# Kernel tuning notes

Hardware: AMD Instinct MI355X
Metric: run time of the kernel (lower is better)

## Reference

```python
import jax, jax.numpy as jnp
import numpy as np

MAX_W = 32  # static upper bound on window length (= max(ends - begins) in the torch code)


def setup_inputs() -> dict:
    key = jax.random.key(0)
    k1, k2, k3 = jax.random.split(key, 3)
    B, T, D, S = 8, 4096, 256, 1024
    features = jax.random.normal(k1, (B, T, D), dtype=jnp.float32)
    begins = jax.random.randint(k2, (B, S), 0, T - MAX_W)
    wins = jax.random.randint(k3, (B, S), 1, MAX_W + 1)
    ends = begins + wins
    return {"features": features, "begins": begins, "ends": ends}


def reference(features, begins, ends):
    # Pooler(mode='mean', dropout_p=0.0) ragged branch: for each span s in batch b,
    # mean of features[b, begins[b,s]:ends[b,s], :] (empty spans -> 0, matching
    # F.embedding_bag mean on an empty bag).
    B, T, D = features.shape
    begins = jnp.maximum(begins, 0)  # clamp_min(0) as in torch code
    ends = jnp.maximum(ends, 0)
    pos = begins[..., None] + jnp.arange(MAX_W)        # [B, S, W]
    valid = pos < ends[..., None]                      # [B, S, W]
    idx = jnp.clip(pos, 0, T - 1)
    gathered = jax.vmap(lambda f, i: f[i])(features, idx)   # [B, S, W, D]
    summed = jnp.sum(jnp.where(valid[..., None], gathered, 0.0), axis=2)  # [B, S, D]
    count = valid.sum(-1).astype(features.dtype)       # [B, S]
    return summed / jnp.maximum(count, 1.0)[..., None]
```

## Files before the change

### kernel.cpp

```cpp
#include <hip/hip_runtime.h>
#include <hip/hip_bf16.h>


#define B_DIM 8
#define T_DIM 4096
#define D_DIM 256
#define S_DIM 1024
#define MAX_W 32
#define RWIDTH 128
#define NBLK (B_DIM * (T_DIM / RWIDTH))
#define STAGE_ROWS (RWIDTH + MAX_W - 1)
#define CAP 508

typedef float vfloat4 __attribute__((ext_vector_type(4)));
typedef const __attribute__((address_space(1))) uint32_t* gptr_t;
typedef __attribute__((address_space(3))) uint32_t* lptr_t;

struct SM {
    float rows[STAGE_ROWS][D_DIM];
    int count;
    unsigned short list[CAP];
};

__global__ __launch_bounds__(1024) void pooler_kernel(
    const float* __restrict__ features,
    const int*   __restrict__ begins,
    const int*   __restrict__ ends,
    float*       __restrict__ out)
{
    __shared__ SM sm;

    const int phys = blockIdx.x;
    const int b = phys & 7;
    const int r = phys >> 3;
    const int tid  = threadIdx.x;
    const int wv   = tid >> 6;
    const int lane = tid & 63;

    if (tid == 0) sm.count = 0;
    __syncthreads();

    const int row0  = r * RWIDTH;
    const int nrows = (T_DIM - row0) < STAGE_ROWS ? (T_DIM - row0) : STAGE_ROWS;
    const float* gbase = features + ((size_t)b * T_DIM + row0) * D_DIM + lane * 4;

    #pragma unroll
    for (int c = 0; c < (STAGE_ROWS + 15) / 16; ++c) {
        const int row = c * 16 + wv;
        if (row < nrows) {
            __builtin_amdgcn_global_load_lds(
                (gptr_t)(gbase + (size_t)row * D_DIM),
                (lptr_t)(&sm.rows[row][0]),
                16, 0, 0);
        }
    }

    {
        const int s  = tid;
        int bg = begins[b * S_DIM + s];
        int bgc = bg > 0 ? bg : 0;
        bgc = bgc < (T_DIM - 1) ? bgc : (T_DIM - 1);
        const bool pred = (bgc >> 7) == r;

        const unsigned long long mask = __ballot(pred);
        const int cnt = __popcll(mask);
        int base = 0;
        if (lane == 0 && cnt) base = atomicAdd(&sm.count, cnt);
        base = __shfl(base, 0);
        if (pred) {
            const int pos =
                base + __popcll(mask & ((1ULL << lane) - 1ULL));
            if (pos < CAP) {
                sm.list[pos] = (unsigned short)s;
            } else {
                int en = ends[b * S_DIM + s];
                int bb = bg > 0 ? bg : 0;
                en = en > 0 ? en : 0;
                en = en < T_DIM ? en : T_DIM;
                int w = en - bb;
                w = w < MAX_W ? w : MAX_W;
                float* op = out + (size_t)(b * S_DIM + s) * D_DIM;
                if (w <= 0) {
                    for (int d = 0; d < D_DIM; ++d) op[d] = 0.f;
                } else {
                    const float* fp =
                        features + ((size_t)b * T_DIM + bb) * D_DIM;
                    const float inv = 1.0f / (float)w;
                    for (int d = 0; d < D_DIM; ++d) {
                        float a = 0.f;
                        for (int j = 0; j < w; ++j) a += fp[(size_t)j * D_DIM + d];
                        op[d] = a * inv;
                    }
                }
            }
        }
    }

    __syncthreads();

    const int cnt = sm.count < CAP ? sm.count : CAP;
    for (int i = wv; i < cnt; i += 16) {
        const int s = sm.list[i];
        int bg = begins[b * S_DIM + s];
        int en = ends[b * S_DIM + s];
        bg = bg > 0 ? bg : 0;
        en = en > 0 ? en : 0;
        en = en < T_DIM ? en : T_DIM;
        int w = en - bg;
        w = w < MAX_W ? w : MAX_W;

        vfloat4* outp =
            reinterpret_cast<vfloat4*>(out + (size_t)(b * S_DIM + s) * D_DIM) + lane;

        if (w <= 0) {
            vfloat4 z = {0.f, 0.f, 0.f, 0.f};
            __builtin_nontemporal_store(z, outp);
            continue;
        }

        const int local = bg - row0;
        const vfloat4* lp =
            reinterpret_cast<const vfloat4*>(&sm.rows[local][0]) + lane;

        vfloat4 acc = {0.f, 0.f, 0.f, 0.f};
        #pragma unroll 8
        for (int j = 0; j < w; ++j) acc += lp[(size_t)j * (D_DIM / 4)];

        const float inv = 1.0f / (float)w;
        vfloat4 res = acc * inv;
        __builtin_nontemporal_store(res, outp);
    }
}

extern "C" void kernel_launch(void* const* d_in, const int* in_sizes, int n_in,
                              void* d_out, int out_size, void* d_ws, size_t ws_size,
                              hipStream_t stream) {
    const float* features = (const float*)d_in[0];
    const int*   begins   = (const int*)d_in[1];
    const int*   ends     = (const int*)d_in[2];
    float*       out      = (float*)d_out;

    pooler_kernel<<<NBLK, 1024, 0, stream>>>(features, begins, ends, out);
}
```

Before: 14.64 us.

## Split staged rows into two halves and overlap second load with first-half pooling

Stages the first 96 rows into LDS, then processes spans whose begin falls in the first 64 rows while the remaining rows load asynchronously. Spans are bucketed into two lists by half, with span id, local offset and width packed into each entry so the compute loop no longer re-reads begins/ends. The goal is to hide part of the global-to-LDS staging latency behind compute. In exchange it adds an extra barrier and vmcnt wait, and CAP shrinks to 120 per half, so a heavier half falls back to the slow per-thread global path more often.

```diff
diff --git a/kernel.cpp b/kernel.cpp
--- a/kernel.cpp
+++ b/kernel.cpp
@@ -10,7 +10,7 @@
 #define RWIDTH 128
 #define NBLK (B_DIM * (T_DIM / RWIDTH))
 #define STAGE_ROWS (RWIDTH + MAX_W - 1)
-#define CAP 508
+#define CAP 120
 
 typedef float vfloat4 __attribute__((ext_vector_type(4)));
 typedef const __attribute__((address_space(1))) uint32_t* gptr_t;
@@ -18,8 +18,8 @@
 
 struct SM {
     float rows[STAGE_ROWS][D_DIM];
-    int count;
-    unsigned short list[CAP];
+    int cnt[2];
+    unsigned int list[2][CAP];
 };
 
 __global__ __launch_bounds__(1024) void pooler_kernel(
@@ -37,7 +37,7 @@
     const int wv   = tid >> 6;
     const int lane = tid & 63;
 
-    if (tid == 0) sm.count = 0;
+    if (tid < 2) sm.cnt[tid] = 0;
     __syncthreads();
 
     const int row0  = r * RWIDTH;
@@ -45,87 +45,122 @@
     const float* gbase = features + ((size_t)b * T_DIM + row0) * D_DIM + lane * 4;
 
     #pragma unroll
-    for (int c = 0; c < (STAGE_ROWS + 15) / 16; ++c) {
-        const int row = c * 16 + wv;
-        if (row < nrows) {
-            __builtin_amdgcn_global_load_lds(
-                (gptr_t)(gbase + (size_t)row * D_DIM),
-                (lptr_t)(&sm.rows[row][0]),
-                16, 0, 0);
-        }
+    for (int k = 0; k < 6; ++k) {
+        const int row = wv + k * 16;
+        __builtin_amdgcn_global_load_lds(
+            (gptr_t)(gbase + (size_t)row * D_DIM),
+            (lptr_t)(&sm.rows[row][0]), 16, 0, 0);
     }
 
     {
-        const int s  = tid;
-        int bg = begins[b * S_DIM + s];
-        int bgc = bg > 0 ? bg : 0;
-        bgc = bgc < (T_DIM - 1) ? bgc : (T_DIM - 1);
+        const int s = tid;
+        const int bg = begins[b * S_DIM + s];
+        const int en = ends[b * S_DIM + s];
+        int begin = bg > 0 ? bg : 0;
+        int end   = en > 0 ? en : 0;
+        end = end < T_DIM ? end : T_DIM;
+        int w = end - begin;
+        w = w < MAX_W ? w : MAX_W;
+        w = w > 0 ? w : 0;
+
+        int bgc = begin < (T_DIM - 1) ? begin : (T_DIM - 1);
         const bool pred = (bgc >> 7) == r;
+        const int half = (bgc >> 6) & 1;
+        const int local = bgc - row0;
 
-        const unsigned long long mask = __ballot(pred);
-        const int cnt = __popcll(mask);
-        int base = 0;
-        if (lane == 0 && cnt) base = atomicAdd(&sm.count, cnt);
-        base = __shfl(base, 0);
-        if (pred) {
-            const int pos =
-                base + __popcll(mask & ((1ULL << lane) - 1ULL));
-            if (pos < CAP) {
-                sm.list[pos] = (unsigned short)s;
-            } else {
-                int en = ends[b * S_DIM + s];
-                int bb = bg > 0 ? bg : 0;
-                en = en > 0 ? en : 0;
-                en = en < T_DIM ? en : T_DIM;
-                int w = en - bb;
-                w = w < MAX_W ? w : MAX_W;
-                float* op = out + (size_t)(b * S_DIM + s) * D_DIM;
-                if (w <= 0) {
-                    for (int d = 0; d < D_DIM; ++d) op[d] = 0.f;
+        #pragma unroll
+        for (int h = 0; h < 2; ++h) {
+            const bool p = pred && (half == h);
+            const unsigned long long mask = __ballot(p);
+            const int c = __popcll(mask);
+            int base = 0;
+            if (lane == 0 && c) base = atomicAdd(&sm.cnt[h], c);
+            base = __shfl(base, 0);
+            if (p) {
+                const int pos = base + __popcll(mask & ((1ULL << lane) - 1ULL));
+                if (pos < CAP) {
+                    sm.list[h][pos] =
+                        (unsigned int)s | ((unsigned int)local << 10)
+                                        | ((unsigned int)w << 17);
                 } else {
-                    const float* fp =
-                        features + ((size_t)b * T_DIM + bb) * D_DIM;
-                    const float inv = 1.0f / (float)w;
-                    for (int d = 0; d < D_DIM; ++d) {
-                        float a = 0.f;
-                        for (int j = 0; j < w; ++j) a += fp[(size_t)j * D_DIM + d];
-                        op[d] = a * inv;
+                    float* op = out + (size_t)(b * S_DIM + s) * D_DIM;
+                    if (w <= 0) {
+                        for (int d = 0; d < D_DIM; ++d) op[d] = 0.f;
+                    } else {
+                        const float* fp =
+                            features + ((size_t)b * T_DIM + begin) * D_DIM;
+                        const float inv = 1.0f / (float)w;
+                        for (int d = 0; d < D_DIM; ++d) {
+                            float a = 0.f;
+                            for (int j = 0; j < w; ++j)
+                                a += fp[(size_t)j * D_DIM + d];
+                            op[d] = a * inv;
+                        }
                     }
                 }
             }
         }
     }
 
+    asm volatile("s_waitcnt vmcnt(0)" ::: "memory");
     __syncthreads();
 
-    const int cnt = sm.count < CAP ? sm.count : CAP;
-    for (int i = wv; i < cnt; i += 16) {
-        const int s = sm.list[i];
-        int bg = begins[b * S_DIM + s];
-        int en = ends[b * S_DIM + s];
-        bg = bg > 0 ? bg : 0;
-        en = en > 0 ? en : 0;
-        en = en < T_DIM ? en : T_DIM;
-        int w = en - bg;
-        w = w < MAX_W ? w : MAX_W;
+    #pragma unroll
+    for (int k = 0; k < 4; ++k) {
+        const int row = 96 + wv + k * 16;
+        if (row < nrows && row < STAGE_ROWS) {
+            __builtin_amdgcn_global_load_lds(
+                (gptr_t)(gbase + (size_t)row * D_DIM),
+                (lptr_t)(&sm.rows[row][0]), 16, 0, 0);
+        }
+    }
 
-        vfloat4* outp =
-            reinterpret_cast<vfloat4*>(out + (size_t)(b * S_DIM + s) * D_DIM) + lane;
+    const int cntA = sm.cnt[0] < CAP ? sm.cnt[0] : CAP;
+    for (int i = wv; i < cntA; i += 16) {
+        const unsigned int e = sm.list[0][i];
+        const int s     = e & 1023;
+        const int local = (e >> 10) & 127;
+        const int w     = (e >> 17) & 63;
 
-        if (w <= 0) {
+        vfloat4* outp = reinterpret_cast<vfloat4*>(
+            out + (size_t)(b * S_DIM + s) * D_DIM) + lane;
+        if (w == 0) {
             vfloat4 z = {0.f, 0.f, 0.f, 0.f};
             __builtin_nontemporal_store(z, outp);
             continue;
         }
-
-        const int local = bg - row0;
         const vfloat4* lp =
             reinterpret_cast<const vfloat4*>(&sm.rows[local][0]) + lane;
-
         vfloat4 acc = {0.f, 0.f, 0.f, 0.f};
         #pragma unroll 8
         for (int j = 0; j < w; ++j) acc += lp[(size_t)j * (D_DIM / 4)];
+        const float inv = 1.0f / (float)w;
+        vfloat4 res = acc * inv;
+        __builtin_nontemporal_store(res, outp);
+    }
 
+    asm volatile("s_waitcnt vmcnt(0)" ::: "memory");
+    __syncthreads();
+
+    const int cntB = sm.cnt[1] < CAP ? sm.cnt[1] : CAP;
+    for (int i = wv; i < cntB; i += 16) {
+        const unsigned int e = sm.list[1][i];
+        const int s     = e & 1023;
+        const int local = (e >> 10) & 127;
+        const int w     = (e >> 17) & 63;
+
+        vfloat4* outp = reinterpret_cast<vfloat4*>(
+            out + (size_t)(b * S_DIM + s) * D_DIM) + lane;
+        if (w == 0) {
+            vfloat4 z = {0.f, 0.f, 0.f, 0.f};
+            __builtin_nontemporal_store(z, outp);
+            continue;
+        }
+        const vfloat4* lp =
+            reinterpret_cast<const vfloat4*>(&sm.rows[local][0]) + lane;
+        vfloat4 acc = {0.f, 0.f, 0.f, 0.f};
+        #pragma unroll 8
+        for (int j = 0; j < w; ++j) acc += lp[(size_t)j * (D_DIM / 4)];
         const float inv = 1.0f / (float)w;
         vfloat4 res = acc * inv;
         __builtin_nontemporal_store(res, outp);
```

Result: faster. 12.91 us (-11.8%).
